# Kernel optimization log

Measured on AMD Instinct MI355X. Metric: run time of the kernel, lower is better.

Reference implementation:

```python
import jax, jax.numpy as jnp
import numpy as np

BATCH = 64
IN_VECN = 1024
IN_VECL = 64
OUT_VECN = 64
OUT_VECL = 32
ROUTINGS = 3
EPS = 1e-5


def squash(x, axis=-1, eps=EPS):
    # squash(x) = |x|^2/(1+|x|^2) * x/(|x|+eps), matching the torch source
    n = jnp.linalg.norm(x, axis=axis, keepdims=True)
    n2 = n * n
    return n2 / (1.0 + n2) * x / (n + eps)


def setup_inputs() -> dict:
    key = jax.random.key(0)
    k1, k2, k3 = jax.random.split(key, 3)
    stdv = 1.0 / np.sqrt(IN_VECN * IN_VECL)  # reset_parameters: uniform(-stdv, stdv)
    u = jax.random.normal(k1, (BATCH, IN_VECN, IN_VECL), dtype=jnp.float32)
    weight = jax.random.uniform(k2, (IN_VECN, OUT_VECN, OUT_VECL, IN_VECL),
                                dtype=jnp.float32, minval=-stdv, maxval=stdv)
    bias = jax.random.uniform(k3, (IN_VECN, OUT_VECN, OUT_VECL),
                              dtype=jnp.float32, minval=-stdv, maxval=stdv)
    return {"u": u, "weight": weight, "bias": bias}


def reference(u, weight, bias):
    # u: [B, N, I]; weight: [N, O, L, I]; bias: [N, O, L]
    # u_hat: [B, N, O, L] -- per-input-capsule prediction for each output capsule
    u_hat = jnp.einsum('bni,noli->bnol', u, weight) + bias[None]
    # retain_grad=False: routing uses detached u_hat
    ud = jax.lax.stop_gradient(u_hat)
    # initial c = softmax(zeros) over out_vecn -> uniform 1/O, shape [1,1,O,1]
    c = jnp.full((1, 1, OUT_VECN, 1), 1.0 / OUT_VECN, dtype=u.dtype)
    b = jnp.zeros((u.shape[0], IN_VECN, OUT_VECN, 1), dtype=u.dtype)
    for _ in range(ROUTINGS - 1):
        v = squash(jnp.sum(ud * c, axis=-3), axis=-1)        # [B, O, L]
        b = b + jnp.sum(ud * v[:, None], axis=-1, keepdims=True)  # [B, N, O, 1]
        c = jax.nn.softmax(b, axis=-2)                        # softmax over O
    return squash(jnp.sum(u_hat * c, axis=-3), axis=-1)      # [B, O, L]
```

## Files before the change

kernel.cpp:

```cpp
#include <hip/hip_runtime.h>

#define NIN 1024
#define IVL 64
#define ONUM 64
#define LVL 32
#define OLSZ 2048

typedef __attribute__((ext_vector_type(4))) float f32x4;
typedef __attribute__((ext_vector_type(4))) unsigned u32x4;
typedef __attribute__((ext_vector_type(8))) short short8;

static __device__ __forceinline__ unsigned short f2bf(float f) {
  unsigned u = __builtin_bit_cast(unsigned, f);
  u += 0x7fffu + ((u >> 16) & 1u);
  return (unsigned short)(u >> 16);
}
static __device__ __forceinline__ float bf2f_lo(unsigned x) {
  return __builtin_bit_cast(float, x << 16);
}
static __device__ __forceinline__ float bf2f_hi(unsigned x) {
  return __builtin_bit_cast(float, x & 0xffff0000u);
}

#define W_BURST16(W, q0, q1, q2, q3)                                     \
  asm volatile(                                                          \
      "global_load_dwordx4 %[w0], %[a0], off nt\n\t"                     \
      "global_load_dwordx4 %[w1], %[a0], off offset:16 nt\n\t"           \
      "global_load_dwordx4 %[w2], %[a0], off offset:128 nt\n\t"          \
      "global_load_dwordx4 %[w3], %[a0], off offset:144 nt\n\t"          \
      "global_load_dwordx4 %[w4], %[a1], off nt\n\t"                     \
      "global_load_dwordx4 %[w5], %[a1], off offset:16 nt\n\t"           \
      "global_load_dwordx4 %[w6], %[a1], off offset:128 nt\n\t"          \
      "global_load_dwordx4 %[w7], %[a1], off offset:144 nt\n\t"          \
      "global_load_dwordx4 %[w8], %[a2], off nt\n\t"                     \
      "global_load_dwordx4 %[w9], %[a2], off offset:16 nt\n\t"           \
      "global_load_dwordx4 %[w10], %[a2], off offset:128 nt\n\t"         \
      "global_load_dwordx4 %[w11], %[a2], off offset:144 nt\n\t"         \
      "global_load_dwordx4 %[w12], %[a3], off nt\n\t"                    \
      "global_load_dwordx4 %[w13], %[a3], off offset:16 nt\n\t"          \
      "global_load_dwordx4 %[w14], %[a3], off offset:128 nt\n\t"         \
      "global_load_dwordx4 %[w15], %[a3], off offset:144 nt\n\t"         \
      : [w0] "=&v"(W[0]), [w1] "=&v"(W[1]), [w2] "=&v"(W[2]),            \
        [w3] "=&v"(W[3]), [w4] "=&v"(W[4]), [w5] "=&v"(W[5]),            \
        [w6] "=&v"(W[6]), [w7] "=&v"(W[7]), [w8] "=&v"(W[8]),            \
        [w9] "=&v"(W[9]), [w10] "=&v"(W[10]), [w11] "=&v"(W[11]),        \
        [w12] "=&v"(W[12]), [w13] "=&v"(W[13]), [w14] "=&v"(W[14]),      \
        [w15] "=&v"(W[15])                                               \
      : [a0] "v"(q0), [a1] "v"(q1), [a2] "v"(q2), [a3] "v"(q3)           \
      : "memory")

#define VM_WAIT16                                       \
  do {                                                  \
    asm volatile("s_waitcnt vmcnt(16)" ::: "memory");   \
    __builtin_amdgcn_sched_barrier(0);                  \
  } while (0)
#define VM_WAIT8                                        \
  do {                                                  \
    asm volatile("s_waitcnt vmcnt(8)" ::: "memory");    \
    __builtin_amdgcn_sched_barrier(0);                  \
  } while (0)

#define TILE(W, TL, C, O0, O1, O2, O3, O4, O5, O6, O7)                        \
  do {                                                                        \
    const f32x4 A0 = (W)[(TL) * 4 + 0];                                       \
    const f32x4 A1 = (W)[(TL) * 4 + 1];                                       \
    const f32x4 A2 = (W)[(TL) * 4 + 2];                                       \
    const f32x4 A3 = (W)[(TL) * 4 + 3];                                       \
    short8 wf0, wf1;                                                          \
    wf0[0] = (short)f2bf(A0[0]); wf0[1] = (short)f2bf(A0[1]);                 \
    wf0[2] = (short)f2bf(A0[2]); wf0[3] = (short)f2bf(A0[3]);                 \
    wf0[4] = (short)f2bf(A1[0]); wf0[5] = (short)f2bf(A1[1]);                 \
    wf0[6] = (short)f2bf(A1[2]); wf0[7] = (short)f2bf(A1[3]);                 \
    wf1[0] = (short)f2bf(A2[0]); wf1[1] = (short)f2bf(A2[1]);                 \
    wf1[2] = (short)f2bf(A2[2]); wf1[3] = (short)f2bf(A2[3]);                 \
    wf1[4] = (short)f2bf(A3[0]); wf1[5] = (short)f2bf(A3[1]);                 \
    wf1[6] = (short)f2bf(A3[2]); wf1[7] = (short)f2bf(A3[3]);                 \
    float4 bf = *(const float4*)&bias_lds[wave * 256 + (C) * 64 + (TL) * 16 + \
                                          quad * 4];                          \
    f32x4 a0 = (f32x4){0.f, 0.f, 0.f, 0.f};                                   \
    f32x4 a1 = a0, a2 = a0, a3 = a0;                                          \
    a0 = __builtin_amdgcn_mfma_f32_16x16x32_bf16(wf0, uf[0][0], a0, 0, 0, 0); \
    a0 = __builtin_amdgcn_mfma_f32_16x16x32_bf16(wf1, uf[0][1], a0, 0, 0, 0); \
    a1 = __builtin_amdgcn_mfma_f32_16x16x32_bf16(wf0, uf[1][0], a1, 0, 0, 0); \
    a1 = __builtin_amdgcn_mfma_f32_16x16x32_bf16(wf1, uf[1][1], a1, 0, 0, 0); \
    a2 = __builtin_amdgcn_mfma_f32_16x16x32_bf16(wf0, uf[2][0], a2, 0, 0, 0); \
    a2 = __builtin_amdgcn_mfma_f32_16x16x32_bf16(wf1, uf[2][1], a2, 0, 0, 0); \
    a3 = __builtin_amdgcn_mfma_f32_16x16x32_bf16(wf0, uf[3][0], a3, 0, 0, 0); \
    a3 = __builtin_amdgcn_mfma_f32_16x16x32_bf16(wf1, uf[3][1], a3, 0, 0, 0); \
    O0 = f2bf(a0[0] + bf.x) | ((unsigned)f2bf(a0[1] + bf.y) << 16);           \
    O1 = f2bf(a0[2] + bf.z) | ((unsigned)f2bf(a0[3] + bf.w) << 16);           \
    O2 = f2bf(a1[0] + bf.x) | ((unsigned)f2bf(a1[1] + bf.y) << 16);           \
    O3 = f2bf(a1[2] + bf.z) | ((unsigned)f2bf(a1[3] + bf.w) << 16);           \
    O4 = f2bf(a2[0] + bf.x) | ((unsigned)f2bf(a2[1] + bf.y) << 16);           \
    O5 = f2bf(a2[2] + bf.z) | ((unsigned)f2bf(a2[3] + bf.w) << 16);           \
    O6 = f2bf(a3[0] + bf.x) | ((unsigned)f2bf(a3[1] + bf.y) << 16);           \
    O7 = f2bf(a3[2] + bf.z) | ((unsigned)f2bf(a3[3] + bf.w) << 16);           \
  } while (0)

#define STEP(W, C)                                                            \
  do {                                                                        \
    u32x4 kA0, kA1, kA2, kA3, kB0, kB1, kB2, kB3;                             \
    TILE(W, 0, C, kA0.x, kA0.y, kA1.x, kA1.y, kA2.x, kA2.y, kA3.x, kA3.y);    \
    TILE(W, 1, C, kA0.z, kA0.w, kA1.z, kA1.w, kA2.z, kA2.w, kA3.z, kA3.w);    \
    TILE(W, 2, C, kB0.x, kB0.y, kB1.x, kB1.y, kB2.x, kB2.y, kB3.x, kB3.y);    \
    TILE(W, 3, C, kB0.z, kB0.w, kB1.z, kB1.w, kB2.z, kB2.w, kB3.z, kB3.w);    \
    const unsigned short* c0 = sb0 + (C) * 64;                                \
    const unsigned short* c1 = sb1 + (C) * 64;                                \
    const unsigned short* c2 = sb2 + (C) * 64;                                \
    const unsigned short* c3 = sb3 + (C) * 64;                                \
    asm volatile(                                                             \
        "global_store_dwordx4 %[a0], %[d0], off\n\t"                          \
        "global_store_dwordx4 %[a0], %[d1], off offset:16\n\t"                \
        "global_store_dwordx4 %[a1], %[d2], off\n\t"                          \
        "global_store_dwordx4 %[a1], %[d3], off offset:16\n\t"                \
        "global_store_dwordx4 %[a2], %[d4], off\n\t"                          \
        "global_store_dwordx4 %[a2], %[d5], off offset:16\n\t"                \
        "global_store_dwordx4 %[a3], %[d6], off\n\t"                          \
        "global_store_dwordx4 %[a3], %[d7], off offset:16\n\t"                \
        :: [a0] "v"(c0), [a1] "v"(c1), [a2] "v"(c2), [a3] "v"(c3),            \
           [d0] "v"(kA0), [d1] "v"(kB0), [d2] "v"(kA1), [d3] "v"(kB1),        \
           [d4] "v"(kA2), [d5] "v"(kB2), [d6] "v"(kA3), [d7] "v"(kB3)         \
        : "memory");                                                          \
  } while (0)

__global__ __launch_bounds__(256, 2) void k_gemm(
    const float* __restrict__ u, const float* __restrict__ w,
    const float* __restrict__ bias, unsigned short* __restrict__ uhat,
    float* __restrict__ szero) {
  const int n = blockIdx.x;
  const int half = blockIdx.y;
  __shared__ __align__(16) unsigned short a_lds[64 * 72];
  __shared__ __align__(16) float bias_lds[1024];
  const int t = threadIdx.x;
  const int lane = t & 63;
  const int wave = t >> 6;
  const int row16 = lane & 15;
  const int quad = lane >> 4;

  {
    const int bid = half * 1024 + n;
    if (t < 192) szero[bid * 192 + t] = 0.f;
  }

  {
    const int b = t >> 2;
    const int i0 = (t & 3) * 16;
    const float* src = u + (size_t)b * (NIN * IVL) + (size_t)n * IVL + i0;
    unsigned short* dst = a_lds + b * 72 + i0;
#pragma unroll
    for (int q = 0; q < 4; ++q) {
      float4 v = *(const float4*)(src + q * 4);
      dst[q * 4 + 0] = f2bf(v.x);
      dst[q * 4 + 1] = f2bf(v.y);
      dst[q * 4 + 2] = f2bf(v.z);
      dst[q * 4 + 3] = f2bf(v.w);
    }
    *(float4*)&bias_lds[t * 4] =
        *(const float4*)(bias + (size_t)n * OLSZ + half * 1024 + t * 4);
  }

  const float* wp = w + (size_t)n * (OLSZ * IVL) +
                    (size_t)(half * 1024 + wave * 256 + row16) * IVL + quad * 8;
  f32x4 bufA[16], bufB[16];
  W_BURST16(bufA, wp, wp + 1024, wp + 2048, wp + 3072);
  W_BURST16(bufB, wp + 4096, wp + 5120, wp + 6144, wp + 7168);

  asm volatile("s_waitcnt lgkmcnt(0)" ::: "memory");
  __builtin_amdgcn_s_barrier();

  short8 uf[4][2];
#pragma unroll
  for (int bt = 0; bt < 4; ++bt) {
#pragma unroll
    for (int ks = 0; ks < 2; ++ks) {
      uf[bt][ks] =
          *(const short8*)(a_lds + (bt * 16 + row16) * 72 + ks * 32 + quad * 8);
    }
  }

  const unsigned short* sb0 = uhat + ((size_t)row16 * NIN + n) * OLSZ +
                              half * 1024 + wave * 256 + quad * 16;
  const unsigned short* sb1 = sb0 + (size_t)16 * NIN * OLSZ;
  const unsigned short* sb2 = sb0 + (size_t)32 * NIN * OLSZ;
  const unsigned short* sb3 = sb0 + (size_t)48 * NIN * OLSZ;

  VM_WAIT16; STEP(bufA, 0); W_BURST16(bufA, wp + 8192, wp + 9216, wp + 10240, wp + 11264);
  VM_WAIT16; STEP(bufB, 1); W_BURST16(bufB, wp + 12288, wp + 13312, wp + 14336, wp + 15360);
  VM_WAIT16; STEP(bufA, 2);
  VM_WAIT8;  STEP(bufB, 3);
}

__global__ __launch_bounds__(256) void k_sum_n(
    const unsigned short* __restrict__ uhat, float* __restrict__ s1) {
  const int b = blockIdx.x >> 5;
  const int chunk = blockIdx.x & 31;
  const int t = threadIdx.x;
  const unsigned short* base =
      uhat + ((size_t)b * NIN + (size_t)chunk * 32) * OLSZ + t * 8;
  float acc[8];
#pragma unroll
  for (int j = 0; j < 8; ++j) acc[j] = 0.f;
#pragma unroll 4
  for (int k = 0; k < 32; ++k) {
    uint4 p = *(const uint4*)(base + (size_t)k * OLSZ);
    unsigned xs[4] = {p.x, p.y, p.z, p.w};
#pragma unroll
    for (int h = 0; h < 4; ++h) {
      acc[2 * h] += bf2f_lo(xs[h]);
      acc[2 * h + 1] += bf2f_hi(xs[h]);
    }
  }
  float* s = s1 + (size_t)b * OLSZ + t * 8;
#pragma unroll
  for (int j = 0; j < 8; ++j) atomicAdd(s + j, acc[j]);
}

__global__ __launch_bounds__(256) void k_route(
    const unsigned short* __restrict__ uhat, const float* __restrict__ svA,
    float scaleA, const float* __restrict__ svB, float scaleB, int useB,
    float* __restrict__ sout) {
  const int b = blockIdx.x >> 5;
  const int chunk = blockIdx.x & 31;
  const int t = threadIdx.x;
  const int lane = t & 63;
  const int wave = t >> 6;
  __shared__ float red[4][OLSZ];

  float v[4][8];
#pragma unroll
  for (int q = 0; q < 4; ++q) {
    const float* svp = svA + (size_t)b * OLSZ + q * 512 + lane * 8;
    float4 a0 = *(const float4*)svp;
    float4 a1 = *(const float4*)(svp + 4);
    v[q][0] = a0.x * scaleA; v[q][1] = a0.y * scaleA;
    v[q][2] = a0.z * scaleA; v[q][3] = a0.w * scaleA;
    v[q][4] = a1.x * scaleA; v[q][5] = a1.y * scaleA;
    v[q][6] = a1.z * scaleA; v[q][7] = a1.w * scaleA;
    float p = 0.f;
#pragma unroll
    for (int j = 0; j < 8; ++j) p = fmaf(v[q][j], v[q][j], p);
    p += __shfl_xor(p, 2);
    p += __shfl_xor(p, 4);
    float f = p / ((1.f + p) * (sqrtf(p) + 1e-5f));
#pragma unroll
    for (int j = 0; j < 8; ++j) v[q][j] *= f;
  }
  if (useB) {
#pragma unroll
    for (int q = 0; q < 4; ++q) {
      const float* svp = svB + (size_t)b * OLSZ + q * 512 + lane * 8;
      float4 a0 = *(const float4*)svp;
      float4 a1 = *(const float4*)(svp + 4);
      float w2[8];
      w2[0] = a0.x * scaleB; w2[1] = a0.y * scaleB;
      w2[2] = a0.z * scaleB; w2[3] = a0.w * scaleB;
      w2[4] = a1.x * scaleB; w2[5] = a1.y * scaleB;
      w2[6] = a1.z * scaleB; w2[7] = a1.w * scaleB;
      float p = 0.f;
#pragma unroll
      for (int j = 0; j < 8; ++j) p = fmaf(w2[j], w2[j], p);
      p += __shfl_xor(p, 2);
      p += __shfl_xor(p, 4);
      float f = p / ((1.f + p) * (sqrtf(p) + 1e-5f));
#pragma unroll
      for (int j = 0; j < 8; ++j) v[q][j] = fmaf(w2[j], f, v[q][j]);
    }
  }

  float racc[4][8];
#pragma unroll
  for (int q = 0; q < 4; ++q)
#pragma unroll
    for (int j = 0; j < 8; ++j) racc[q][j] = 0.f;

  const int n0 = chunk * 32 + wave * 8;
  const unsigned short* ub = uhat + ((size_t)b * NIN + n0) * OLSZ + lane * 8;

  uint4 pA[4], pB[4];
#pragma unroll
  for (int q = 0; q < 4; ++q) pA[q] = *(const uint4*)(ub + q * 512);

  auto process = [&](const uint4(&pk)[4]) {
    float ud[4][8];
    float d[4];
#pragma unroll
    for (int q = 0; q < 4; ++q) {
      unsigned xs[4] = {pk[q].x, pk[q].y, pk[q].z, pk[q].w};
#pragma unroll
      for (int h = 0; h < 4; ++h) {
        ud[q][2 * h] = bf2f_lo(xs[h]);
        ud[q][2 * h + 1] = bf2f_hi(xs[h]);
      }
      float p = 0.f;
#pragma unroll
      for (int j = 0; j < 8; ++j) p = fmaf(ud[q][j], v[q][j], p);
      p += __shfl_xor(p, 2);
      p += __shfl_xor(p, 4);
      d[q] = p;
    }
    float m = fmaxf(fmaxf(d[0], d[1]), fmaxf(d[2], d[3]));
    m = fmaxf(m, __shfl_xor(m, 1));
    m = fmaxf(m, __shfl_xor(m, 8));
    m = fmaxf(m, __shfl_xor(m, 16));
    m = fmaxf(m, __shfl_xor(m, 32));
    float e0 = __expf(d[0] - m);
    float e1 = __expf(d[1] - m);
    float e2 = __expf(d[2] - m);
    float e3 = __expf(d[3] - m);
    float ls = (e0 + e1) + (e2 + e3);
    ls += __shfl_xor(ls, 1);
    ls += __shfl_xor(ls, 8);
    ls += __shfl_xor(ls, 16);
    ls += __shfl_xor(ls, 32);
    float inv = 1.0f / ls;
    float c[4] = {e0 * inv, e1 * inv, e2 * inv, e3 * inv};
#pragma unroll
    for (int q = 0; q < 4; ++q) {
#pragma unroll
      for (int j = 0; j < 8; ++j)
        racc[q][j] = fmaf(c[q], ud[q][j], racc[q][j]);
    }
  };

#pragma unroll
  for (int kk = 0; kk < 4; ++kk) {
    {
#pragma unroll
      for (int q = 0; q < 4; ++q)
        pB[q] = *(const uint4*)(ub + (size_t)(2 * kk + 1) * OLSZ + q * 512);
    }
    process(pA);
    if (2 * kk + 2 < 8) {
#pragma unroll
      for (int q = 0; q < 4; ++q)
        pA[q] = *(const uint4*)(ub + (size_t)(2 * kk + 2) * OLSZ + q * 512);
    }
    process(pB);
  }

#pragma unroll
  for (int q = 0; q < 4; ++q) {
    float* dst = &red[wave][q * 512 + lane * 8];
    *(float4*)(dst) =
        make_float4(racc[q][0], racc[q][1], racc[q][2], racc[q][3]);
    *(float4*)(dst + 4) =
        make_float4(racc[q][4], racc[q][5], racc[q][6], racc[q][7]);
  }
  __syncthreads();
  float* so = sout + (size_t)b * OLSZ;
#pragma unroll
  for (int j = 0; j < 8; ++j) {
    const int idx = t + 256 * j;
    float s = (red[0][idx] + red[1][idx]) + (red[2][idx] + red[3][idx]);
    atomicAdd(so + idx, s);
  }
}

__global__ __launch_bounds__(256) void k_final(const float* __restrict__ s3,
                                               float* __restrict__ out) {
  const int b = blockIdx.x;
  const int t = threadIdx.x;
  __shared__ float norm2[64];
  if (t < 64) norm2[t] = 0.f;
  __syncthreads();
  float scv[8];
#pragma unroll
  for (int k = 0; k < 8; ++k) {
    int idx = t + k * 256;
    float sc = s3[b * OLSZ + idx];
    scv[k] = sc;
    int o = ((idx >> 9) << 4) + (((idx >> 6) & 7) << 1) + ((idx >> 3) & 1);
    atomicAdd(&norm2[o], sc * sc);
  }
  __syncthreads();
#pragma unroll
  for (int k = 0; k < 8; ++k) {
    int idx = t + k * 256;
    int o = ((idx >> 9) << 4) + (((idx >> 6) & 7) << 1) + ((idx >> 3) & 1);
    float n2 = norm2[o];
    float f = n2 / ((1.f + n2) * (sqrtf(n2) + 1e-5f));
    int q2 = (idx >> 4) & 3;
    int t2 = (idx >> 2) & 3;
    int j = idx & 3;
    int fr = (idx & ~63) | (t2 << 4) | (q2 << 2) | j;
    out[b * OLSZ + fr] = scv[k] * f;
  }
}

extern "C" void kernel_launch(void* const* d_in, const int* in_sizes, int n_in,
                              void* d_out, int out_size, void* d_ws,
                              size_t ws_size, hipStream_t stream) {
  const float* u = (const float*)d_in[0];
  const float* w = (const float*)d_in[1];
  const float* bias = (const float*)d_in[2];
  float* out = (float*)d_out;

  char* ws = (char*)d_ws;
  unsigned short* uhat = (unsigned short*)ws;
  float* s1 = (float*)(ws + (size_t)268435456);
  float* s2 = s1 + 131072;
  float* s3 = s2 + 131072;

  k_gemm<<<dim3(1024, 2), dim3(256), 0, stream>>>(u, w, bias, uhat, s1);
  k_sum_n<<<dim3(2048), dim3(256), 0, stream>>>(uhat, s1);
  k_route<<<dim3(2048), dim3(256), 0, stream>>>(uhat, s1, 1.0f / 64.0f,
                                                (const float*)nullptr, 0.f, 0, s2);
  k_route<<<dim3(2048), dim3(256), 0, stream>>>(uhat, s1, 1.0f / 64.0f,
                                                s2, 1.0f, 1, s3);
  k_final<<<dim3(64), dim3(256), 0, stream>>>(s3, out);
}
```

Measured before the change: 503.9 us.

## Store u_hat in [N][B] order and drop nontemporal hints on weight loads

Result: faster. 433.8 us, median of 2 (-13.9%).

```diff
diff --git a/kernel.cpp b/kernel.cpp
--- a/kernel.cpp
+++ b/kernel.cpp
@@ -24,22 +24,22 @@
 
 #define W_BURST16(W, q0, q1, q2, q3)                                     \
   asm volatile(                                                          \
-      "global_load_dwordx4 %[w0], %[a0], off nt\n\t"                     \
-      "global_load_dwordx4 %[w1], %[a0], off offset:16 nt\n\t"           \
-      "global_load_dwordx4 %[w2], %[a0], off offset:128 nt\n\t"          \
-      "global_load_dwordx4 %[w3], %[a0], off offset:144 nt\n\t"          \
-      "global_load_dwordx4 %[w4], %[a1], off nt\n\t"                     \
-      "global_load_dwordx4 %[w5], %[a1], off offset:16 nt\n\t"           \
-      "global_load_dwordx4 %[w6], %[a1], off offset:128 nt\n\t"          \
-      "global_load_dwordx4 %[w7], %[a1], off offset:144 nt\n\t"          \
-      "global_load_dwordx4 %[w8], %[a2], off nt\n\t"                     \
-      "global_load_dwordx4 %[w9], %[a2], off offset:16 nt\n\t"           \
-      "global_load_dwordx4 %[w10], %[a2], off offset:128 nt\n\t"         \
-      "global_load_dwordx4 %[w11], %[a2], off offset:144 nt\n\t"         \
-      "global_load_dwordx4 %[w12], %[a3], off nt\n\t"                    \
-      "global_load_dwordx4 %[w13], %[a3], off offset:16 nt\n\t"          \
-      "global_load_dwordx4 %[w14], %[a3], off offset:128 nt\n\t"         \
-      "global_load_dwordx4 %[w15], %[a3], off offset:144 nt\n\t"         \
+      "global_load_dwordx4 %[w0], %[a0], off\n\t"                        \
+      "global_load_dwordx4 %[w1], %[a0], off offset:16\n\t"              \
+      "global_load_dwordx4 %[w2], %[a0], off offset:128\n\t"             \
+      "global_load_dwordx4 %[w3], %[a0], off offset:144\n\t"             \
+      "global_load_dwordx4 %[w4], %[a1], off\n\t"                        \
+      "global_load_dwordx4 %[w5], %[a1], off offset:16\n\t"              \
+      "global_load_dwordx4 %[w6], %[a1], off offset:128\n\t"             \
+      "global_load_dwordx4 %[w7], %[a1], off offset:144\n\t"             \
+      "global_load_dwordx4 %[w8], %[a2], off\n\t"                        \
+      "global_load_dwordx4 %[w9], %[a2], off offset:16\n\t"              \
+      "global_load_dwordx4 %[w10], %[a2], off offset:128\n\t"            \
+      "global_load_dwordx4 %[w11], %[a2], off offset:144\n\t"            \
+      "global_load_dwordx4 %[w12], %[a3], off\n\t"                       \
+      "global_load_dwordx4 %[w13], %[a3], off offset:16\n\t"             \
+      "global_load_dwordx4 %[w14], %[a3], off offset:128\n\t"            \
+      "global_load_dwordx4 %[w15], %[a3], off offset:144\n\t"            \
       : [w0] "=&v"(W[0]), [w1] "=&v"(W[1]), [w2] "=&v"(W[2]),            \
         [w3] "=&v"(W[3]), [w4] "=&v"(W[4]), [w5] "=&v"(W[5]),            \
         [w6] "=&v"(W[6]), [w7] "=&v"(W[7]), [w8] "=&v"(W[8]),            \
@@ -178,11 +178,11 @@
     }
   }
 
-  const unsigned short* sb0 = uhat + ((size_t)row16 * NIN + n) * OLSZ +
+  const unsigned short* sb0 = uhat + ((size_t)n * 64 + row16) * OLSZ +
                               half * 1024 + wave * 256 + quad * 16;
-  const unsigned short* sb1 = sb0 + (size_t)16 * NIN * OLSZ;
-  const unsigned short* sb2 = sb0 + (size_t)32 * NIN * OLSZ;
-  const unsigned short* sb3 = sb0 + (size_t)48 * NIN * OLSZ;
+  const unsigned short* sb1 = sb0 + (size_t)16 * OLSZ;
+  const unsigned short* sb2 = sb0 + (size_t)32 * OLSZ;
+  const unsigned short* sb3 = sb0 + (size_t)48 * OLSZ;
 
   VM_WAIT16; STEP(bufA, 0); W_BURST16(bufA, wp + 8192, wp + 9216, wp + 10240, wp + 11264);
   VM_WAIT16; STEP(bufB, 1); W_BURST16(bufB, wp + 12288, wp + 13312, wp + 14336, wp + 15360);
@@ -192,17 +192,17 @@
 
 __global__ __launch_bounds__(256) void k_sum_n(
     const unsigned short* __restrict__ uhat, float* __restrict__ s1) {
-  const int b = blockIdx.x >> 5;
-  const int chunk = blockIdx.x & 31;
+  const int b = blockIdx.x >> 3;
+  const int nc = blockIdx.x & 7;
   const int t = threadIdx.x;
   const unsigned short* base =
-      uhat + ((size_t)b * NIN + (size_t)chunk * 32) * OLSZ + t * 8;
+      uhat + ((size_t)(nc * 128) * 64 + b) * OLSZ + t * 8;
   float acc[8];
 #pragma unroll
   for (int j = 0; j < 8; ++j) acc[j] = 0.f;
 #pragma unroll 4
-  for (int k = 0; k < 32; ++k) {
-    uint4 p = *(const uint4*)(base + (size_t)k * OLSZ);
+  for (int k = 0; k < 128; ++k) {
+    uint4 p = *(const uint4*)(base + (size_t)k * 64 * OLSZ);
     unsigned xs[4] = {p.x, p.y, p.z, p.w};
 #pragma unroll
     for (int h = 0; h < 4; ++h) {
@@ -274,7 +274,8 @@
     for (int j = 0; j < 8; ++j) racc[q][j] = 0.f;
 
   const int n0 = chunk * 32 + wave * 8;
-  const unsigned short* ub = uhat + ((size_t)b * NIN + n0) * OLSZ + lane * 8;
+  const unsigned short* ub = uhat + ((size_t)n0 * 64 + b) * OLSZ + lane * 8;
+  const size_t NSTRIDE = (size_t)64 * OLSZ;
 
   uint4 pA[4], pB[4];
 #pragma unroll
@@ -327,13 +328,13 @@
     {
 #pragma unroll
       for (int q = 0; q < 4; ++q)
-        pB[q] = *(const uint4*)(ub + (size_t)(2 * kk + 1) * OLSZ + q * 512);
+        pB[q] = *(const uint4*)(ub + (size_t)(2 * kk + 1) * NSTRIDE + q * 512);
     }
     process(pA);
     if (2 * kk + 2 < 8) {
 #pragma unroll
       for (int q = 0; q < 4; ++q)
-        pA[q] = *(const uint4*)(ub + (size_t)(2 * kk + 2) * OLSZ + q * 512);
+        pA[q] = *(const uint4*)(ub + (size_t)(2 * kk + 2) * NSTRIDE + q * 512);
     }
     process(pB);
   }
@@ -402,7 +403,7 @@
   float* s3 = s2 + 131072;
 
   k_gemm<<<dim3(1024, 2), dim3(256), 0, stream>>>(u, w, bias, uhat, s1);
-  k_sum_n<<<dim3(2048), dim3(256), 0, stream>>>(uhat, s1);
+  k_sum_n<<<dim3(512), dim3(256), 0, stream>>>(uhat, s1);
   k_route<<<dim3(2048), dim3(256), 0, stream>>>(uhat, s1, 1.0f / 64.0f,
                                                 (const float*)nullptr, 0.f, 0, s2);
   k_route<<<dim3(2048), dim3(256), 0, stream>>>(uhat, s1, 1.0f / 64.0f,
```
